# Performance work log

Measured on AMD Instinct MI355X. Metric: run time of the kernel, lower is better.

Reference implementation:

```python
import jax, jax.numpy as jnp
import numpy as np

V, E, H, L, S, T = 100000, 256, 512, 50000, 512, 64


def setup_inputs() -> dict:
    key = jax.random.key(0)
    ks = jax.random.split(key, 14)
    s = 0.02
    return {
        "encoder_outputs": jax.random.normal(ks[0], (1, S, H), jnp.float32),
        "enc_h0": jax.random.normal(ks[1], (1, 1, H), jnp.float32),
        "enc_c0": jax.random.normal(ks[2], (1, 1, H), jnp.float32),
        "emb_table": jax.random.normal(ks[3], (V, E), jnp.float32) * s,
        "W_attn": jax.random.normal(ks[4], (H, E), jnp.float32) * s,
        "b_attn": jnp.zeros((H,), jnp.float32),
        "W_ih": jax.random.normal(ks[5], (4 * H, H), jnp.float32) * s,
        "W_hh": jax.random.normal(ks[6], (4 * H, H), jnp.float32) * s,
        "b_ih": jnp.zeros((4 * H,), jnp.float32),
        "b_hh": jnp.zeros((4 * H,), jnp.float32),
        "W_out": jax.random.normal(ks[7], (L, H), jnp.float32) * s,
        "b_out": jnp.zeros((L,), jnp.float32),
        "word_inputs": jax.random.randint(ks[8], (T,), 0, V),
        "labels": jax.random.randint(ks[9], (T,), 0, L),
    }


def reference(encoder_outputs, enc_h0, enc_c0, emb_table, W_attn, b_attn,
              W_ih, W_hh, b_ih, b_hh, W_out, b_out, word_inputs, labels):
    # batch == 1 throughout (matches forward_train); dropout is identity (eval).
    enc = encoder_outputs[0]          # [S, H]
    h0 = enc_h0[0, 0]                 # [H]  (bidirect hidden already flattened to 1x1xH)
    c0 = enc_c0[0, 0]                 # [H]

    def step(carry, xs):
        h, c = carry
        widx, label = xs
        e = emb_table[widx]                               # [E]   embedding lookup
        q = W_attn @ e + b_attn                           # [H]   attn projection (Linear)
        alphas = jax.nn.softmax(enc @ q)                  # [S]   bmm + softmax
        ctx = alphas @ enc                                # [H]   bmm -> context
        # single-step LSTM (PyTorch gate order: i, f, g, o)
        gates = W_ih @ ctx + b_ih + W_hh @ h + b_hh       # [4H]
        i, f, g, o = jnp.split(gates, 4)
        i = jax.nn.sigmoid(i); f = jax.nn.sigmoid(f)
        g = jnp.tanh(g);       o = jax.nn.sigmoid(o)
        c2 = f * c + i * g
        h2 = o * jnp.tanh(c2)
        logits = W_out @ h2 + b_out                       # [L]   hidden2tag
        ls = jax.nn.log_softmax(logits)
        # NLLLoss(ignore_index=0, reduction='sum')
        step_loss = jnp.where(label == 0, jnp.float32(0.0), -ls[label])
        return (h2, c2), step_loss

    (_, _), losses = jax.lax.scan(step, (h0, c0),
                                  (word_inputs, labels))
    return jnp.sum(losses)
```

## Files before the change

kernel.cpp:

```cpp
#include <hip/hip_runtime.h>
#include <hip/hip_bf16.h>

#define V_ 100000
#define E_ 256
#define H_ 512
#define L_ 50000
#define S_ 512
#define T_ 64
#define NB_ 782
#define NBP_ 784
#define NWG_ 32
#define NPF_ 128

typedef short bf16x8 __attribute__((ext_vector_type(8)));
typedef float f32x4 __attribute__((ext_vector_type(4)));

__device__ __forceinline__ float sigm(float x){ return 1.0f/(1.0f+__expf(-x)); }
__device__ __forceinline__ float tanh_fast(float x){
    x = fminf(fmaxf(x, -15.f), 15.f);
    float e = __expf(2.f * x);
    return __fdividef(e - 1.f, e + 1.f);
}
__device__ __forceinline__ unsigned bf16rne(float x){
    unsigned u = __float_as_uint(x);
    return (u + 0x7fffu + ((u >> 16) & 1u)) >> 16;
}
__device__ __forceinline__ float bcast(float v, int l){
    return __uint_as_float(__builtin_amdgcn_readlane(__float_as_uint(v), l));
}

__global__ __launch_bounds__(256) void k_attn(
    const float* __restrict__ enc, const float* __restrict__ emb,
    const float* __restrict__ W_attn, const float* __restrict__ b_attn,
    const int* __restrict__ word_inputs, float* __restrict__ ctx_out)
{
    __shared__ float e_l[E_];
    __shared__ float q_l[H_];
    __shared__ float sc[S_];
    __shared__ float red[8];
    const int t = blockIdx.x, tid = threadIdx.x;
    const int widx = word_inputs[t];

    e_l[tid] = emb[(long)widx * E_ + tid];
    __syncthreads();

    for (int rr = 0; rr < 2; ++rr) {
        int r = tid + rr * 256;
        const float4* wrow = (const float4*)(W_attn + r * E_);
        const float4* ev = (const float4*)e_l;
        float acc = b_attn[r];
        #pragma unroll 8
        for (int j = 0; j < E_ / 4; ++j) {
            float4 w = wrow[j], e4 = ev[j];
            acc += w.x*e4.x + w.y*e4.y + w.z*e4.z + w.w*e4.w;
        }
        q_l[r] = acc;
    }
    __syncthreads();

    for (int rr = 0; rr < 2; ++rr) {
        int s = tid + rr * 256;
        const float4* er = (const float4*)(enc + s * H_);
        const float4* qv = (const float4*)q_l;
        float acc = 0.f;
        #pragma unroll 8
        for (int j = 0; j < H_ / 4; ++j) {
            float4 a = er[j], b = qv[j];
            acc += a.x*b.x + a.y*b.y + a.z*b.z + a.w*b.w;
        }
        sc[s] = acc;
    }
    __syncthreads();

    float m = fmaxf(sc[tid], sc[tid + 256]);
    for (int off = 32; off; off >>= 1) m = fmaxf(m, __shfl_down(m, off));
    if ((tid & 63) == 0) red[tid >> 6] = m;
    __syncthreads();
    if (tid == 0) red[4] = fmaxf(fmaxf(red[0], red[1]), fmaxf(red[2], red[3]));
    __syncthreads();
    m = red[4];
    float e0 = __expf(sc[tid] - m), e1 = __expf(sc[tid + 256] - m);
    sc[tid] = e0; sc[tid + 256] = e1;
    float ssum = e0 + e1;
    for (int off = 32; off; off >>= 1) ssum += __shfl_down(ssum, off);
    if ((tid & 63) == 0) red[tid >> 6] = ssum;
    __syncthreads();
    if (tid == 0) red[5] = red[0] + red[1] + red[2] + red[3];
    __syncthreads();
    float inv = 1.0f / red[5];

    for (int rr = 0; rr < 2; ++rr) {
        int h = tid + rr * 256;
        float acc = 0.f;
        #pragma unroll 4
        for (int s = 0; s < S_; ++s) acc += sc[s] * enc[s * H_ + h];
        ctx_out[t * H_ + h] = acc * inv;
    }
}

__global__ __launch_bounds__(256) void k_gatepre(
    const float* __restrict__ ctx, const float* __restrict__ W_ih,
    const float* __restrict__ b_ih, const float* __restrict__ b_hh,
    float* __restrict__ A_pre)
{
    __shared__ float ctx_t[H_ * 65];
    __shared__ float w_l[8 * H_];
    const int tid = threadIdx.x;
    const int r0 = blockIdx.x * 8;

    for (int i = 0; i < 32; ++i) {
        int p = tid + i * 256;
        int t = p >> 7, k4 = p & 127;
        float4 v = ((const float4*)ctx)[p];
        ctx_t[(k4*4+0)*65 + t] = v.x;
        ctx_t[(k4*4+1)*65 + t] = v.y;
        ctx_t[(k4*4+2)*65 + t] = v.z;
        ctx_t[(k4*4+3)*65 + t] = v.w;
    }
    for (int i = 0; i < 4; ++i) {
        int p = tid + i * 256;
        int row = p >> 7, k4 = p & 127;
        float4 v = ((const float4*)W_ih)[(r0 + row) * (H_/4) + k4];
        float* dst = &w_l[row * H_ + k4 * 4];
        dst[0]=v.x; dst[1]=v.y; dst[2]=v.z; dst[3]=v.w;
    }
    __syncthreads();

    const int t = tid & 63, half = tid >> 6;
    const float* w0 = &w_l[(half*2+0) * H_];
    const float* w1 = &w_l[(half*2+1) * H_];
    float acc0 = 0.f, acc1 = 0.f;
    #pragma unroll 4
    for (int k = 0; k < H_; ++k) {
        float cv = ctx_t[k * 65 + t];
        acc0 += w0[k] * cv;
        acc1 += w1[k] * cv;
    }
    int ra = r0 + half * 2, rb = ra + 1;
    A_pre[t * 2048 + ra] = acc0 + b_ih[ra] + b_hh[ra];
    A_pre[t * 2048 + rb] = acc1 + b_ih[rb] + b_hh[rb];
}

#define ST(i, val) asm volatile("v_accvgpr_write_b32 %0, %1" : "=a"(g##i) : "v"(val));
#define STQ(q,i0,i1,i2,i3) { float4 v_ = wsrc[q]; ST(i0,v_.x) ST(i1,v_.y) ST(i2,v_.z) ST(i3,v_.w) }
#define MAC4(i0,i1,i2,i3) { float w0_,w1_,w2_,w3_; \
  asm volatile("v_accvgpr_read_b32 %0, %1" : "=v"(w0_) : "a"(g##i0)); \
  asm volatile("v_accvgpr_read_b32 %0, %1" : "=v"(w1_) : "a"(g##i1)); \
  asm volatile("v_accvgpr_read_b32 %0, %1" : "=v"(w2_) : "a"(g##i2)); \
  asm volatile("v_accvgpr_read_b32 %0, %1" : "=v"(w3_) : "a"(g##i3)); \
  a0 += w0_ * bcast(hv, i0); a1 += w1_ * bcast(hv, i1); \
  a2 += w2_ * bcast(hv, i2); a3 += w3_ * bcast(hv, i3); }

__global__ __launch_bounds__(512, 1) void k_lstm(
    const float* __restrict__ W_hh, const float* __restrict__ A_pre,
    const float* __restrict__ h0, const float* __restrict__ c0,
    float* __restrict__ h_buf, const float* __restrict__ W_out)
{
    const int tid = threadIdx.x, wg = blockIdx.x;

    if (wg >= NWG_) {
        const long total = (long)L_ * H_ / 4;
        const long stride = (long)NPF_ * 512;
        const float4* src = (const float4*)W_out;
        float acc = 0.f;
        for (long i = (long)(wg - NWG_) * 512 + tid; i < total; i += stride) {
            float4 v = src[i];
            acc += v.x + v.y + v.z + v.w;
        }
        asm volatile("" :: "v"(acc));
        return;
    }

    __shared__ float A_l[T_ * 64];
    __shared__ float red[2][8][64];

    const int base = wg * 16;
    const int lane = tid & 63;
    const int ks   = tid >> 6;
    const int G = ((lane >> 4) << 9) + base + (lane & 15);

    float g0,g1,g2,g3,g4,g5,g6,g7,g8,g9,g10,g11,g12,g13,g14,g15;
    float g16,g17,g18,g19,g20,g21,g22,g23,g24,g25,g26,g27,g28,g29,g30,g31;
    float g32,g33,g34,g35,g36,g37,g38,g39,g40,g41,g42,g43,g44,g45,g46,g47;
    float g48,g49,g50,g51,g52,g53,g54,g55,g56,g57,g58,g59,g60,g61,g62,g63;
    {
        const float4* wsrc = (const float4*)(W_hh + (long)G * H_ + ks * 64);
        STQ(0,0,1,2,3)     STQ(1,4,5,6,7)     STQ(2,8,9,10,11)   STQ(3,12,13,14,15)
        STQ(4,16,17,18,19) STQ(5,20,21,22,23) STQ(6,24,25,26,27) STQ(7,28,29,30,31)
        STQ(8,32,33,34,35) STQ(9,36,37,38,39) STQ(10,40,41,42,43)STQ(11,44,45,46,47)
        STQ(12,48,49,50,51)STQ(13,52,53,54,55)STQ(14,56,57,58,59)STQ(15,60,61,62,63)
    }

    for (int i = 0; i < 8; ++i) {
        int p = tid + i * 512;
        int tt = p >> 6, rr = p & 63;
        A_l[p] = A_pre[tt * 2048 + ((rr >> 4) << 9) + base + (rr & 15)];
    }
    float c_reg = 0.f;
    if (tid < 16) c_reg = c0[base + tid];
    __syncthreads();

    const unsigned SENT = 0xFFFFFFFFu;

    for (int t = 0; t < T_; ++t) {
        float hv;
        if (t == 0) {
            hv = h0[ks * 64 + lane];
        } else {
            const unsigned* hb = (const unsigned*)h_buf + (t - 1) * H_ + ks * 64;
            unsigned u = __hip_atomic_load(hb + lane, __ATOMIC_RELAXED,
                                           __HIP_MEMORY_SCOPE_AGENT);
            while (u == SENT) {
                __builtin_amdgcn_s_sleep(1);
                u = __hip_atomic_load(hb + lane, __ATOMIC_RELAXED,
                                      __HIP_MEMORY_SCOPE_AGENT);
            }
            hv = __uint_as_float(u);
        }

        float a0 = 0.f, a1 = 0.f, a2 = 0.f, a3 = 0.f;
        MAC4(0,1,2,3)     MAC4(4,5,6,7)     MAC4(8,9,10,11)   MAC4(12,13,14,15)
        MAC4(16,17,18,19) MAC4(20,21,22,23) MAC4(24,25,26,27) MAC4(28,29,30,31)
        MAC4(32,33,34,35) MAC4(36,37,38,39) MAC4(40,41,42,43) MAC4(44,45,46,47)
        MAC4(48,49,50,51) MAC4(52,53,54,55) MAC4(56,57,58,59) MAC4(60,61,62,63)
        red[t & 1][ks][lane] = (a0 + a1) + (a2 + a3);
        __syncthreads();

        if (ks == 0) {
            float s = A_l[t * 64 + lane];
            #pragma unroll
            for (int k2 = 0; k2 < 8; ++k2) s += red[t & 1][k2][lane];
            float gf_ = __shfl_down(s, 16);
            float gg_ = __shfl_down(s, 32);
            float go_ = __shfl_down(s, 48);
            if (lane < 16) {
                float gi = sigm(s);
                float gf = sigm(gf_);
                float gg = tanh_fast(gg_);
                float go = sigm(go_);
                float c2 = gf * c_reg + gi * gg;
                c_reg = c2;
                float h2 = go * tanh_fast(c2);
                __hip_atomic_store((unsigned*)h_buf + t * H_ + base + lane,
                                   __float_as_uint(h2),
                                   __ATOMIC_RELAXED, __HIP_MEMORY_SCOPE_AGENT);
            }
        }
    }
}

__global__ __launch_bounds__(256) void k_out(
    const float* __restrict__ W_out, const float* __restrict__ b_out,
    const float* __restrict__ h_buf, const int* __restrict__ labels,
    float* __restrict__ pm, float* __restrict__ ps, float* __restrict__ ll)
{
    __shared__ __align__(16) unsigned char smem[65536];
    const int tid = threadIdx.x;
    const int r0 = blockIdx.x * 64;
    const int lane = tid & 63, w = tid >> 6;
    const int g = lane >> 4, li = lane & 15;

    for (int i = 0; i < 32; ++i) {
        int p = tid + i * 256;
        int t = p >> 7, k4 = p & 127;
        float4 v = ((const float4*)h_buf)[p];
        unsigned p01 = bf16rne(v.x) | (bf16rne(v.y) << 16);
        unsigned p23 = bf16rne(v.z) | (bf16rne(v.w) << 16);
        unsigned byte = (unsigned)(t * 1024 + k4 * 8) ^ ((unsigned)(t & 7) << 4);
        *(uint2*)(smem + byte) = make_uint2(p01, p23);
    }

    f32x4 acc0 = {0.f,0.f,0.f,0.f}, acc1 = {0.f,0.f,0.f,0.f};
    f32x4 acc2 = {0.f,0.f,0.f,0.f}, acc3 = {0.f,0.f,0.f,0.f};
    __syncthreads();

    int rrow = r0 + w * 16 + li;
    int rw = rrow < L_ ? rrow : (L_ - 1);
    const float* ap = W_out + (long)rw * H_ + g * 8;

    #pragma unroll
    for (int kk = 0; kk < 16; ++kk) {
        float4 va = *(const float4*)(ap + kk * 32);
        float4 vb = *(const float4*)(ap + kk * 32 + 4);
        union { unsigned u[4]; bf16x8 v; } A;
        A.u[0] = bf16rne(va.x) | (bf16rne(va.y) << 16);
        A.u[1] = bf16rne(va.z) | (bf16rne(va.w) << 16);
        A.u[2] = bf16rne(vb.x) | (bf16rne(vb.y) << 16);
        A.u[3] = bf16rne(vb.z) | (bf16rne(vb.w) << 16);

        #pragma unroll
        for (int nt = 0; nt < 4; ++nt) {
            int t = nt * 16 + li;
            unsigned byte = (unsigned)(t * 1024 + kk * 64 + g * 16)
                          ^ ((unsigned)(t & 7) << 4);
            bf16x8 B = *(const bf16x8*)(smem + byte);
            f32x4* accp = (nt == 0) ? &acc0 : (nt == 1) ? &acc1
                        : (nt == 2) ? &acc2 : &acc3;
            *accp = __builtin_amdgcn_mfma_f32_16x16x32_bf16(A.v, B, *accp, 0, 0, 0);
        }
    }
    __syncthreads();

    float* lg   = (float*)smem;
    float* redb = (float*)(smem + 64 * 65 * 4);
    float* gmax = redb + 256;

    #pragma unroll
    for (int nt = 0; nt < 4; ++nt) {
        const f32x4 a = (nt == 0) ? acc0 : (nt == 1) ? acc1
                      : (nt == 2) ? acc2 : acc3;
        int t = nt * 16 + li;
        #pragma unroll
        for (int q = 0; q < 4; ++q) {
            int rloc = w * 16 + g * 4 + q;
            int r = r0 + rloc;
            float v = -1e30f;
            if (r < L_) v = a[q] + b_out[r];
            lg[rloc * 65 + t] = v;
        }
    }
    __syncthreads();

    const int t = tid & 63, part = tid >> 6;
    float m = -1e30f;
    #pragma unroll
    for (int r16 = 0; r16 < 16; ++r16)
        m = fmaxf(m, lg[(part*16 + r16)*65 + t]);
    redb[part*64 + t] = m;
    __syncthreads();
    if (part == 0)
        gmax[t] = fmaxf(fmaxf(redb[t], redb[64+t]), fmaxf(redb[128+t], redb[192+t]));
    __syncthreads();
    float gm = gmax[t];
    float s = 0.f;
    #pragma unroll
    for (int r16 = 0; r16 < 16; ++r16)
        s += __expf(lg[(part*16 + r16)*65 + t] - gm);
    __syncthreads();
    redb[part*64 + t] = s;
    __syncthreads();
    if (part == 0) {
        pm[t * NBP_ + blockIdx.x] = gm;
        ps[t * NBP_ + blockIdx.x] = redb[t] + redb[64+t] + redb[128+t] + redb[192+t];
        int lb = labels[t];
        if (lb >= r0 && lb < r0 + 64) ll[t] = lg[(lb - r0)*65 + t];
    }
}

__global__ __launch_bounds__(256) void k_final(
    const float* __restrict__ pm, const float* __restrict__ ps,
    const float* __restrict__ ll, const int* __restrict__ labels,
    float* __restrict__ out)
{
    __shared__ float rbuf[8];
    const int t = blockIdx.x, tid = threadIdx.x;
    float m = -1e30f;
    for (int b = tid; b < NB_; b += 256) m = fmaxf(m, pm[t * NBP_ + b]);
    for (int off = 32; off; off >>= 1) m = fmaxf(m, __shfl_down(m, off));
    if ((tid & 63) == 0) rbuf[tid >> 6] = m;
    __syncthreads();
    if (tid == 0) rbuf[4] = fmaxf(fmaxf(rbuf[0], rbuf[1]), fmaxf(rbuf[2], rbuf[3]));
    __syncthreads();
    float M = rbuf[4];
    __syncthreads();
    float s = 0.f;
    for (int b = tid; b < NB_; b += 256)
        s += ps[t * NBP_ + b] * __expf(pm[t * NBP_ + b] - M);
    for (int off = 32; off; off >>= 1) s += __shfl_down(s, off);
    if ((tid & 63) == 0) rbuf[tid >> 6] = s;
    __syncthreads();
    if (tid == 0) {
        float S = rbuf[0] + rbuf[1] + rbuf[2] + rbuf[3];
        int lb = labels[t];
        if (lb != 0) {
            float loss = -(ll[t] - M - __logf(S));
            atomicAdd(out, loss);
        }
    }
}

extern "C" void kernel_launch(void* const* d_in, const int* in_sizes, int n_in,
                              void* d_out, int out_size, void* d_ws, size_t ws_size,
                              hipStream_t stream)
{
    (void)in_sizes; (void)n_in; (void)out_size; (void)ws_size;
    const float* enc    = (const float*)d_in[0];
    const float* h0     = (const float*)d_in[1];
    const float* c0     = (const float*)d_in[2];
    const float* emb    = (const float*)d_in[3];
    const float* W_attn = (const float*)d_in[4];
    const float* b_attn = (const float*)d_in[5];
    const float* W_ih   = (const float*)d_in[6];
    const float* W_hh   = (const float*)d_in[7];
    const float* b_ih   = (const float*)d_in[8];
    const float* b_hh   = (const float*)d_in[9];
    const float* W_out  = (const float*)d_in[10];
    const float* b_out  = (const float*)d_in[11];
    const int* widx     = (const int*)d_in[12];
    const int* labels   = (const int*)d_in[13];
    float* out = (float*)d_out;

    char* ws = (char*)d_ws;
    float* ctx   = (float*)(ws + 0);
    float* A_pre = (float*)(ws + 131072);
    float* h_buf = (float*)(ws + 655360);
    float* pm    = (float*)(ws + 786688);
    float* ps    = (float*)(ws + 987392);
    float* ll    = (float*)(ws + 1188096);

    hipMemsetAsync(h_buf, 0xFF, T_ * H_ * sizeof(float), stream);
    hipMemsetAsync(out, 0, sizeof(float), stream);

    k_attn<<<T_, 256, 0, stream>>>(enc, emb, W_attn, b_attn, widx, ctx);
    k_gatepre<<<256, 256, 0, stream>>>(ctx, W_ih, b_ih, b_hh, A_pre);
    k_lstm<<<NWG_ + NPF_, 512, 0, stream>>>(W_hh, A_pre, h0, c0, h_buf, W_out);
    k_out<<<NB_, 256, 0, stream>>>(W_out, b_out, h_buf, labels, pm, ps, ll);
    k_final<<<T_, 256, 0, stream>>>(pm, ps, ll, labels, out);
}
```

Measured before the change: 251.9 us.

## Drop W_out L2-prefetch blocks and hoist AGPR weight reads before h wait

Removes the 128 extra workgroups that streamed W_out through cache during the sequential LSTM kernel. It also moves all AGPR-to-VGPR weight reads to the top of each timestep, ahead of the spin-wait on the previous hidden state, with a scheduling barrier. Hoisting the reads takes them off the critical path after h arrives, but needs 64 more live VGPRs. Dropping the prefetch lowers memory contention during the recurrence, but k_out may then read W_out cold from HBM.

```diff
diff --git a/kernel.cpp b/kernel.cpp
--- a/kernel.cpp
+++ b/kernel.cpp
@@ -10,7 +10,6 @@
 #define NB_ 782
 #define NBP_ 784
 #define NWG_ 32
-#define NPF_ 128
 
 typedef short bf16x8 __attribute__((ext_vector_type(8)));
 typedef float f32x4 __attribute__((ext_vector_type(4)));
@@ -143,33 +142,18 @@
 
 #define ST(i, val) asm volatile("v_accvgpr_write_b32 %0, %1" : "=a"(g##i) : "v"(val));
 #define STQ(q,i0,i1,i2,i3) { float4 v_ = wsrc[q]; ST(i0,v_.x) ST(i1,v_.y) ST(i2,v_.z) ST(i3,v_.w) }
-#define MAC4(i0,i1,i2,i3) { float w0_,w1_,w2_,w3_; \
-  asm volatile("v_accvgpr_read_b32 %0, %1" : "=v"(w0_) : "a"(g##i0)); \
-  asm volatile("v_accvgpr_read_b32 %0, %1" : "=v"(w1_) : "a"(g##i1)); \
-  asm volatile("v_accvgpr_read_b32 %0, %1" : "=v"(w2_) : "a"(g##i2)); \
-  asm volatile("v_accvgpr_read_b32 %0, %1" : "=v"(w3_) : "a"(g##i3)); \
-  a0 += w0_ * bcast(hv, i0); a1 += w1_ * bcast(hv, i1); \
-  a2 += w2_ * bcast(hv, i2); a3 += w3_ * bcast(hv, i3); }
+#define RD1(i) float wv##i; asm volatile("v_accvgpr_read_b32 %0, %1" : "=v"(wv##i) : "a"(g##i));
+#define RD4(i0,i1,i2,i3) RD1(i0) RD1(i1) RD1(i2) RD1(i3)
+#define FMA4(i0,i1,i2,i3) \
+    a0 += wv##i0 * bcast(hv, i0); a1 += wv##i1 * bcast(hv, i1); \
+    a2 += wv##i2 * bcast(hv, i2); a3 += wv##i3 * bcast(hv, i3);
 
 __global__ __launch_bounds__(512, 1) void k_lstm(
     const float* __restrict__ W_hh, const float* __restrict__ A_pre,
     const float* __restrict__ h0, const float* __restrict__ c0,
-    float* __restrict__ h_buf, const float* __restrict__ W_out)
+    float* __restrict__ h_buf)
 {
     const int tid = threadIdx.x, wg = blockIdx.x;
-
-    if (wg >= NWG_) {
-        const long total = (long)L_ * H_ / 4;
-        const long stride = (long)NPF_ * 512;
-        const float4* src = (const float4*)W_out;
-        float acc = 0.f;
-        for (long i = (long)(wg - NWG_) * 512 + tid; i < total; i += stride) {
-            float4 v = src[i];
-            acc += v.x + v.y + v.z + v.w;
-        }
-        asm volatile("" :: "v"(acc));
-        return;
-    }
 
     __shared__ float A_l[T_ * 64];
     __shared__ float red[2][8][64];
@@ -203,6 +187,12 @@
     const unsigned SENT = 0xFFFFFFFFu;
 
     for (int t = 0; t < T_; ++t) {
+        RD4(0,1,2,3)     RD4(4,5,6,7)     RD4(8,9,10,11)   RD4(12,13,14,15)
+        RD4(16,17,18,19) RD4(20,21,22,23) RD4(24,25,26,27) RD4(28,29,30,31)
+        RD4(32,33,34,35) RD4(36,37,38,39) RD4(40,41,42,43) RD4(44,45,46,47)
+        RD4(48,49,50,51) RD4(52,53,54,55) RD4(56,57,58,59) RD4(60,61,62,63)
+        __builtin_amdgcn_sched_barrier(0);
+
         float hv;
         if (t == 0) {
             hv = h0[ks * 64 + lane];
@@ -219,10 +209,10 @@
         }
 
         float a0 = 0.f, a1 = 0.f, a2 = 0.f, a3 = 0.f;
-        MAC4(0,1,2,3)     MAC4(4,5,6,7)     MAC4(8,9,10,11)   MAC4(12,13,14,15)
-        MAC4(16,17,18,19) MAC4(20,21,22,23) MAC4(24,25,26,27) MAC4(28,29,30,31)
-        MAC4(32,33,34,35) MAC4(36,37,38,39) MAC4(40,41,42,43) MAC4(44,45,46,47)
-        MAC4(48,49,50,51) MAC4(52,53,54,55) MAC4(56,57,58,59) MAC4(60,61,62,63)
+        FMA4(0,1,2,3)     FMA4(4,5,6,7)     FMA4(8,9,10,11)   FMA4(12,13,14,15)
+        FMA4(16,17,18,19) FMA4(20,21,22,23) FMA4(24,25,26,27) FMA4(28,29,30,31)
+        FMA4(32,33,34,35) FMA4(36,37,38,39) FMA4(40,41,42,43) FMA4(44,45,46,47)
+        FMA4(48,49,50,51) FMA4(52,53,54,55) FMA4(56,57,58,59) FMA4(60,61,62,63)
         red[t & 1][ks][lane] = (a0 + a1) + (a2 + a3);
         __syncthreads();
 
@@ -413,7 +403,7 @@
 
     k_attn<<<T_, 256, 0, stream>>>(enc, emb, W_attn, b_attn, widx, ctx);
     k_gatepre<<<256, 256, 0, stream>>>(ctx, W_ih, b_ih, b_hh, A_pre);
-    k_lstm<<<NWG_ + NPF_, 512, 0, stream>>>(W_hh, A_pre, h0, c0, h_buf, W_out);
+    k_lstm<<<NWG_, 512, 0, stream>>>(W_hh, A_pre, h0, c0, h_buf);
     k_out<<<NB_, 256, 0, stream>>>(W_out, b_out, h_buf, labels, pm, ps, ll);
     k_final<<<T_, 256, 0, stream>>>(pm, ps, ll, labels, out);
 }
```

New measurement: 240.1 us. 1.05x faster.
